# Kernel optimization log

Hardware: AMD Instinct MI355X
Metric: run time of the kernel (lower is better)

Reference implementation:

```python
import jax, jax.numpy as jnp
import numpy as np

M, N = 128, 128          # SOM grid
NITER = 1000             # total training iterations
ALPHA = 0.3              # base learning rate (torch default)
SIGMA = max(M, N) / 2.0  # base neighbourhood radius (torch default)
BS, DIM = 4096, 768


def setup_inputs() -> dict:
    key = jax.random.key(0)
    k1, k2 = jax.random.split(key)
    embedded = jax.random.normal(k1, (BS, DIM), dtype=jnp.float32)   # SapBERT CLS reps
    weights = jax.random.normal(k2, (M * N, DIM), dtype=jnp.float32)  # codebook / SOM weights
    return {"embedded": embedded, "weights": weights, "it": 100}


def reference(embedded, weights, it):
    comps = weights.shape[0]
    # neuron grid locations [comps, 2] (row-major i,j like neuron_locations())
    locs = jnp.stack(
        jnp.meshgrid(jnp.arange(M), jnp.arange(N), indexing="ij"), axis=-1
    ).reshape(comps, 2).astype(jnp.float32)

    # BMU search: squared Euclidean distances (argmin identical to argmin of sqrt)
    # [bs, comps] — avoids materializing the torch [bs, comps, dim] repeat
    d2 = (
        jnp.sum(embedded * embedded, axis=1)[:, None]
        + jnp.sum(weights * weights, axis=1)[None, :]
        - 2.0 * (embedded @ weights.T)
    )
    bmu_index = jnp.argmin(d2, axis=1)          # [bs]
    bmu_loc = locs[bmu_index]                   # [bs, 2] gather

    # linearly decaying learning rate / sigma
    decay = 1.0 - it / NITER
    alpha_op = ALPHA * decay
    sigma_op = SIGMA * decay

    # Gaussian neighbourhood over grid distances [bs, comps]
    grid_d2 = jnp.sum((locs[None, :, :] - bmu_loc[:, None, :]) ** 2, axis=-1)
    lr = alpha_op * jnp.exp(-grid_d2 / (sigma_op * sigma_op))

    # delta[c,d] = sum_b lr[b,c] * (x[b,d] - w[c,d])  (no bs x comps x dim materialization)
    delta = jnp.einsum("bc,bd->cd", lr, embedded) - jnp.sum(lr, axis=0)[:, None] * weights
    return weights + delta
```

## Files before the change

### kernel.cpp

```cpp
#include <hip/hip_runtime.h>
#include <hip/hip_fp16.h>
#include <cstdint>
#include <cstddef>

#define BS    4096
#define DIM   768
#define GM    128
#define GN    128
#define COMPS (GM * GN)
#define NITER_F 1000.0f
#define ALPHA0  0.3f
#define SIGMA0  64.0f

typedef _Float16 half8  __attribute__((ext_vector_type(8)));
typedef _Float16 half4v __attribute__((ext_vector_type(4)));
typedef _Float16 half2v __attribute__((ext_vector_type(2)));
typedef float    floatx4 __attribute__((ext_vector_type(4)));

#define XH_OFF    0UL
#define WH_OFF    (8UL * 1024UL * 1024UL)
#define G_OFF     0UL
#define GH_BYTES  ((size_t)COMPS * DIM * 2UL)
#define BEST_OFF  ((size_t)COMPS * DIM * 4UL)
#define BEST_BYTES ((size_t)BS * 8UL)
#define CNT_OFF   (BEST_OFF + BEST_BYTES)
#define CNT_BYTES ((size_t)COMPS * 4UL)
#define WN2_OFF   (CNT_OFF + CNT_BYTES)

#define GPTR(p) ((const __attribute__((address_space(1))) void*)(p))
#define LPTR(p) ((__attribute__((address_space(3))) void*)(p))

__device__ __forceinline__ unsigned long long packScore(float s, int c) {
    unsigned u = __float_as_uint(s);
    u = (u & 0x80000000u) ? ~u : (u | 0x80000000u);
    return ((unsigned long long)u << 32) | (unsigned)(~(unsigned)c);
}

__device__ __forceinline__ unsigned long long shfl_xor_u64(unsigned long long v, int m) {
    unsigned lo = (unsigned)v, hi = (unsigned)(v >> 32);
    lo = (unsigned)__shfl_xor((int)lo, m, 64);
    hi = (unsigned)__shfl_xor((int)hi, m, 64);
    return ((unsigned long long)hi << 32) | lo;
}

__device__ __forceinline__ void atomicAddPkF16(_Float16* p, half2v v) {
    asm volatile("global_atomic_pk_add_f16 %0, %1, off" : : "v"(p), "v"(v) : "memory");
}

__global__ void cvt_kernel(const float* __restrict__ src, _Float16* __restrict__ dst, int n4) {
    int i = blockIdx.x * 256 + threadIdx.x;
    if (i >= n4) return;
    float4 v = ((const float4*)src)[i];
    half4v h;
    h[0] = (_Float16)v.x; h[1] = (_Float16)v.y;
    h[2] = (_Float16)v.z; h[3] = (_Float16)v.w;
    ((half4v*)dst)[i] = h;
}

__global__ __launch_bounds__(192) void cvtw_wn2_kernel(
    const float* __restrict__ w, _Float16* __restrict__ wh, float* __restrict__ wn2) {
    const int c = blockIdx.x;
    const int t = threadIdx.x;
    const size_t i4 = (size_t)c * 192 + t;
    float4 v = ((const float4*)w)[i4];
    half4v h;
    h[0] = (_Float16)v.x; h[1] = (_Float16)v.y;
    h[2] = (_Float16)v.z; h[3] = (_Float16)v.w;
    ((half4v*)wh)[i4] = h;
    float s = v.x * v.x + v.y * v.y + v.z * v.z + v.w * v.w;
    #pragma unroll
    for (int off = 32; off; off >>= 1) s += __shfl_down(s, off, 64);
    __shared__ float p[3];
    if ((t & 63) == 0) p[t >> 6] = s;
    __syncthreads();
    if (t == 0) wn2[c] = 0.5f * (p[0] + p[1] + p[2]);
}

#define BMU_NT 24

__global__ __launch_bounds__(512, 2) void bmu_kernel(
    const _Float16* __restrict__ xh, const _Float16* __restrict__ wh,
    const float* __restrict__ wn2, unsigned long long* __restrict__ best) {
    __shared__ _Float16 AB[4][2][8192];
    __shared__ unsigned long long red[256];

    const int tid  = threadIdx.x;
    const int wv   = tid >> 6;
    const int lane = tid & 63;
    const int l15  = lane & 15;
    const int q    = lane >> 4;
    const int wr   = wv >> 2;
    const int wc   = wv & 3;

    const int bid = blockIdx.x;
    const int xcd = bid & 7;
    const int rem = bid >> 3;
    const int cbl = rem & 3;
    const int bb  = (rem >> 2) & 15;
    const int cbg = rem >> 6;
    const int cb  = xcd * 8 + cbg * 4 + cbl;
    const int b0 = bb * 256;
    const int c0 = cb * 256;

    if (tid < 256) red[tid] = 0ULL;

    const int Ls = tid >> 3;
    const int ss = tid & 7;
    const int sl = ss ^ (Ls & 7);
    const int prow = 2 * Ls + (sl >> 2);
    const int kc8  = (sl & 3) * 8;
    const _Float16* gA0 = xh + (size_t)(b0 + prow) * DIM + kc8;
    const _Float16* gA1 = gA0 + (size_t)128 * DIM;
    const _Float16* gB0 = wh + (size_t)(c0 + prow) * DIM + kc8;
    const _Float16* gB1 = gB0 + (size_t)128 * DIM;
    const int ldsoff = wv * 512;

    int aoff[8], boff[4];
    #pragma unroll
    for (int i = 0; i < 8; ++i) {
        const int row = wr * 128 + i * 16 + l15;
        const int line = row >> 1;
        const int ps = (((row & 1) << 2) | q) ^ (line & 7);
        aoff[i] = line * 64 + ps * 8;
    }
    #pragma unroll
    for (int jj = 0; jj < 4; ++jj) {
        const int row = wc * 64 + jj * 16 + l15;
        const int line = row >> 1;
        const int ps = (((row & 1) << 2) | q) ^ (line & 7);
        boff[jj] = line * 64 + ps * 8;
    }

    floatx4 acc[8][4];
    #pragma unroll
    for (int i = 0; i < 8; ++i)
        #pragma unroll
        for (int jj = 0; jj < 4; ++jj) acc[i][jj] = (floatx4){0.f, 0.f, 0.f, 0.f};

    #pragma unroll
    for (int t = 0; t < 3; ++t) {
        _Float16* A = &AB[t][0][0];
        _Float16* B = &AB[t][1][0];
        __builtin_amdgcn_global_load_lds(GPTR(gA0 + t * 32), LPTR(A + ldsoff),        16, 0, 0);
        __builtin_amdgcn_global_load_lds(GPTR(gA1 + t * 32), LPTR(A + 4096 + ldsoff), 16, 0, 0);
        __builtin_amdgcn_global_load_lds(GPTR(gB0 + t * 32), LPTR(B + ldsoff),        16, 0, 0);
        __builtin_amdgcn_global_load_lds(GPTR(gB1 + t * 32), LPTR(B + 4096 + ldsoff), 16, 0, 0);
    }

    for (int t = 0; t < BMU_NT; ++t) {
        if (t < BMU_NT - 2)       asm volatile("s_waitcnt vmcnt(8)" ::: "memory");
        else if (t == BMU_NT - 2) asm volatile("s_waitcnt vmcnt(4)" ::: "memory");
        else                      asm volatile("s_waitcnt vmcnt(0)" ::: "memory");
        __builtin_amdgcn_s_barrier();
        asm volatile("" ::: "memory");

        const _Float16* A = &AB[t & 3][0][0];
        const _Float16* B = &AB[t & 3][1][0];
        const bool more = (t + 3) < BMU_NT;
        _Float16* An = &AB[(t + 3) & 3][0][0];
        _Float16* Bn = &AB[(t + 3) & 3][1][0];
        const int t3 = (t + 3) * 32;

        half8 af[8], bf[4];
        #pragma unroll
        for (int i = 0; i < 4; ++i) af[i] = *(const half8*)(A + aoff[i]);
        bf[0] = *(const half8*)(B + boff[0]);
        bf[1] = *(const half8*)(B + boff[1]);
        if (more) __builtin_amdgcn_global_load_lds(GPTR(gA0 + t3), LPTR(An + ldsoff), 16, 0, 0);
        __builtin_amdgcn_s_setprio(1);
        #pragma unroll
        for (int i = 0; i < 4; ++i) {
            acc[i][0] = __builtin_amdgcn_mfma_f32_16x16x32_f16(af[i], bf[0], acc[i][0], 0, 0, 0);
            acc[i][1] = __builtin_amdgcn_mfma_f32_16x16x32_f16(af[i], bf[1], acc[i][1], 0, 0, 0);
        }
        __builtin_amdgcn_s_setprio(0);
        #pragma unroll
        for (int i = 4; i < 8; ++i) af[i] = *(const half8*)(A + aoff[i]);
        if (more) __builtin_amdgcn_global_load_lds(GPTR(gA1 + t3), LPTR(An + 4096 + ldsoff), 16, 0, 0);
        __builtin_amdgcn_s_setprio(1);
        #pragma unroll
        for (int i = 4; i < 8; ++i) {
            acc[i][0] = __builtin_amdgcn_mfma_f32_16x16x32_f16(af[i], bf[0], acc[i][0], 0, 0, 0);
            acc[i][1] = __builtin_amdgcn_mfma_f32_16x16x32_f16(af[i], bf[1], acc[i][1], 0, 0, 0);
        }
        __builtin_amdgcn_s_setprio(0);
        bf[2] = *(const half8*)(B + boff[2]);
        bf[3] = *(const half8*)(B + boff[3]);
        if (more) __builtin_amdgcn_global_load_lds(GPTR(gB0 + t3), LPTR(Bn + ldsoff), 16, 0, 0);
        __builtin_amdgcn_s_setprio(1);
        #pragma unroll
        for (int i = 4; i < 8; ++i) {
            acc[i][2] = __builtin_amdgcn_mfma_f32_16x16x32_f16(af[i], bf[2], acc[i][2], 0, 0, 0);
            acc[i][3] = __builtin_amdgcn_mfma_f32_16x16x32_f16(af[i], bf[3], acc[i][3], 0, 0, 0);
        }
        __builtin_amdgcn_s_setprio(0);
        if (more) __builtin_amdgcn_global_load_lds(GPTR(gB1 + t3), LPTR(Bn + 4096 + ldsoff), 16, 0, 0);
        __builtin_amdgcn_s_setprio(1);
        #pragma unroll
        for (int i = 0; i < 4; ++i) {
            acc[i][2] = __builtin_amdgcn_mfma_f32_16x16x32_f16(af[i], bf[2], acc[i][2], 0, 0, 0);
            acc[i][3] = __builtin_amdgcn_mfma_f32_16x16x32_f16(af[i], bf[3], acc[i][3], 0, 0, 0);
        }
        __builtin_amdgcn_s_setprio(0);
    }

    float wnj[4];
    #pragma unroll
    for (int jj = 0; jj < 4; ++jj) wnj[jj] = wn2[c0 + wc * 64 + jj * 16 + l15];

    #pragma unroll
    for (int i = 0; i < 8; ++i) {
        #pragma unroll
        for (int r = 0; r < 4; ++r) {
            unsigned long long m = 0ULL;
            #pragma unroll
            for (int jj = 0; jj < 4; ++jj) {
                const float s = acc[i][jj][r] - wnj[jj];
                const unsigned long long p = packScore(s, c0 + wc * 64 + jj * 16 + l15);
                if (p > m) m = p;
            }
            #pragma unroll
            for (int msk = 1; msk <= 8; msk <<= 1) {
                const unsigned long long o = shfl_xor_u64(m, msk);
                if (o > m) m = o;
            }
            if (l15 == 0)
                atomicMax(&red[wr * 128 + i * 16 + q * 4 + r], m);
        }
    }
    __syncthreads();
    if (tid < 256) atomicMax(&best[b0 + tid], red[tid]);
}

__global__ void scatter_kernel(const unsigned long long* __restrict__ best,
                               const float* __restrict__ x,
                               _Float16* __restrict__ Gh, float* __restrict__ cnt) {
    const int b = blockIdx.x;
    const int c = (int)(~(unsigned)(best[b] & 0xFFFFFFFFULL));
    _Float16* gr = Gh + (size_t)c * DIM;
    const float2* xr = (const float2*)(x + (size_t)b * DIM);
    #pragma unroll
    for (int u = 0; u < 2; ++u) {
        const int d = threadIdx.x + u * 192;
        const float2 v = xr[d];
        half2v h;
        h[0] = (_Float16)v.x; h[1] = (_Float16)v.y;
        atomicAddPkF16(gr + d * 2, h);
    }
    if (threadIdx.x == 0) atomicAdd(&cnt[c], 1.0f);
}

#define EP 136
#define BP 40

__global__ __launch_bounds__(256) void convA_kernel(
    const _Float16* Gh, _Float16* Hh, const int* __restrict__ itp) {
    __shared__ _Float16 Es[128 * EP];
    __shared__ _Float16 Bs[128 * BP];
    const int d0 = blockIdx.x * 128;
    const int ib = blockIdx.y;
    const int tid = threadIdx.x;
    const int wv = tid >> 6, lane = tid & 63;
    const int l15 = lane & 15, q = lane >> 4;
    const int mrow = (wv >> 1) * 64, ncol = (wv & 1) * 64;

    {
        const float decay = 1.f - (float)(*itp) / NITER_F;
        const float sig = SIGMA0 * decay;
        const float inv = -1.f / (sig * sig);
        const int row = tid >> 1, hh = tid & 1;
        _Float16* dst = Es + row * EP + hh * 64;
        #pragma unroll
        for (int u = 0; u < 64; ++u) {
            const float dd = (float)(row - hh * 64 - u);
            dst[u] = (_Float16)__expf(dd * dd * inv);
        }
    }

    floatx4 acc[4][4];
    #pragma unroll
    for (int i = 0; i < 4; ++i)
        #pragma unroll
        for (int j = 0; j < 4; ++j) acc[i][j] = (floatx4){0.f, 0.f, 0.f, 0.f};

    const int dpo = (tid & 15) * 8;
    const int rsel = tid >> 4;
    const int wsw = ((tid & 15) & 3) << 3;
    for (int k0 = 0; k0 < 128; k0 += 32) {
        __syncthreads();
        #pragma unroll
        for (int s = 0; s < 2; ++s) {
            const int j = k0 + s * 16 + rsel;
            const half8 v = *(const half8*)(Gh + (size_t)(ib * 128 + j) * DIM + d0 + dpo);
            #pragma unroll
            for (int u = 0; u < 8; ++u)
                Bs[(dpo + u) * BP + ((s * 16 + rsel) ^ wsw)] = v[u];
        }
        __syncthreads();
        half8 af[4], bf[4];
        #pragma unroll
        for (int i = 0; i < 4; ++i)
            af[i] = *(const half8*)(Es + (mrow + i * 16 + l15) * EP + k0 + q * 8);
        #pragma unroll
        for (int j = 0; j < 4; ++j) {
            const int row = ncol + j * 16 + l15;
            bf[j] = *(const half8*)(Bs + row * BP + ((q ^ ((row >> 3) & 3)) << 3));
        }
        #pragma unroll
        for (int i = 0; i < 4; ++i)
            #pragma unroll
            for (int j = 0; j < 4; ++j)
                acc[i][j] = __builtin_amdgcn_mfma_f32_16x16x32_f16(af[i], bf[j], acc[i][j], 0, 0, 0);
    }
    __syncthreads();
    float* Ebf = (float*)Es;
    #pragma unroll
    for (int ch = 0; ch < 2; ++ch) {
        if ((wv >> 1) == ch) {
            #pragma unroll
            for (int i = 0; i < 4; ++i)
                #pragma unroll
                for (int j = 0; j < 4; ++j)
                    #pragma unroll
                    for (int r = 0; r < 4; ++r)
                        Ebf[(i * 16 + q * 4 + r) * 132 + ncol + j * 16 + l15] = acc[i][j][r];
        }
        __syncthreads();
        {
            const int row = tid >> 2, seg = tid & 3;
            const int m = ch * 64 + row;
            _Float16* hp = Hh + (size_t)(ib * 128 + m) * DIM + d0 + seg * 32;
            #pragma unroll
            for (int u = 0; u < 4; ++u) {
                const float* sp = Ebf + row * 132 + seg * 32 + u * 8;
                half8 hv;
                #pragma unroll
                for (int e = 0; e < 8; ++e) hv[e] = (_Float16)sp[e];
                *(half8*)(hp + u * 8) = hv;
            }
        }
        __syncthreads();
    }
}

__global__ __launch_bounds__(256) void convB_kernel(
    const _Float16* Hh, const float* __restrict__ w, const float* __restrict__ cnt,
    const int* __restrict__ itp, float* __restrict__ out) {
    __shared__ _Float16 Es[128 * EP];
    __shared__ _Float16 Bs[128 * BP];
    __shared__ float cntHs[128];
    __shared__ float Ss[128];
    const int d0 = blockIdx.x * 128;
    const int jc = blockIdx.y;
    const int tid = threadIdx.x;
    const int wv = tid >> 6, lane = tid & 63;
    const int l15 = lane & 15, q = lane >> 4;
    const int mrow = (wv >> 1) * 64, ncol = (wv & 1) * 64;
    const float decay = 1.f - (float)(*itp) / NITER_F;
    const float alpha = ALPHA0 * decay;
    const float sig = SIGMA0 * decay;
    const float inv = -1.f / (sig * sig);

    if (tid < 128) {
        float s = 0.f;
        for (int j = 0; j < 128; ++j) {
            const float dd = (float)(jc - j);
            s += __expf(dd * dd * inv) * cnt[tid * 128 + j];
        }
        cntHs[tid] = s;
    }
    {
        const int row = tid >> 1, hh = tid & 1;
        _Float16* dst = Es + row * EP + hh * 64;
        #pragma unroll
        for (int u = 0; u < 64; ++u) {
            const float dd = (float)(row - hh * 64 - u);
            dst[u] = (_Float16)__expf(dd * dd * inv);
        }
    }
    __syncthreads();
    if (tid < 128) {
        float s = 0.f;
        for (int i = 0; i < 128; ++i) {
            const float dd = (float)(tid - i);
            s += __expf(dd * dd * inv) * cntHs[i];
        }
        Ss[tid] = s;
    }

    floatx4 acc[4][4];
    #pragma unroll
    for (int i = 0; i < 4; ++i)
        #pragma unroll
        for (int j = 0; j < 4; ++j) acc[i][j] = (floatx4){0.f, 0.f, 0.f, 0.f};

    const int dpo = (tid & 15) * 8;
    const int rsel = tid >> 4;
    const int wsw = ((tid & 15) & 3) << 3;
    for (int k0 = 0; k0 < 128; k0 += 32) {
        __syncthreads();
        #pragma unroll
        for (int s = 0; s < 2; ++s) {
            const int i = k0 + s * 16 + rsel;
            const half8 v = *(const half8*)(Hh + (size_t)(i * 128 + jc) * DIM + d0 + dpo);
            #pragma unroll
            for (int u = 0; u < 8; ++u)
                Bs[(dpo + u) * BP + ((s * 16 + rsel) ^ wsw)] = v[u];
        }
        __syncthreads();
        half8 af[4], bf[4];
        #pragma unroll
        for (int i = 0; i < 4; ++i)
            af[i] = *(const half8*)(Es + (mrow + i * 16 + l15) * EP + k0 + q * 8);
        #pragma unroll
        for (int j = 0; j < 4; ++j) {
            const int row = ncol + j * 16 + l15;
            bf[j] = *(const half8*)(Bs + row * BP + ((q ^ ((row >> 3) & 3)) << 3));
        }
        #pragma unroll
        for (int i = 0; i < 4; ++i)
            #pragma unroll
            for (int j = 0; j < 4; ++j)
                acc[i][j] = __builtin_amdgcn_mfma_f32_16x16x32_f16(af[i], bf[j], acc[i][j], 0, 0, 0);
    }
    __syncthreads();
    float* Ebf = (float*)Es;
    #pragma unroll
    for (int ch = 0; ch < 2; ++ch) {
        if ((wv >> 1) == ch) {
            #pragma unroll
            for (int i = 0; i < 4; ++i)
                #pragma unroll
                for (int j = 0; j < 4; ++j)
                    #pragma unroll
                    for (int r = 0; r < 4; ++r)
                        Ebf[(i * 16 + q * 4 + r) * 132 + ncol + j * 16 + l15] = acc[i][j][r];
        }
        __syncthreads();
        {
            const int row = tid >> 2, seg = tid & 3;
            const int m = ch * 64 + row;
            const int c = m * 128 + jc;
            const float scl = 1.f - alpha * Ss[m];
            const size_t g = (size_t)c * DIM + d0 + seg * 32;
            #pragma unroll
            for (int u = 0; u < 8; ++u) {
                float4 wv4 = *(const float4*)(w + g + u * 4);
                float4 t4  = *(const float4*)(Ebf + row * 132 + seg * 32 + u * 4);
                float4 o;
                o.x = wv4.x * scl + alpha * t4.x;
                o.y = wv4.y * scl + alpha * t4.y;
                o.z = wv4.z * scl + alpha * t4.z;
                o.w = wv4.w * scl + alpha * t4.w;
                *(float4*)(out + g + u * 4) = o;
            }
        }
        __syncthreads();
    }
}

extern "C" void kernel_launch(void* const* d_in, const int* in_sizes, int n_in,
                              void* d_out, int out_size, void* d_ws, size_t ws_size,
                              hipStream_t stream) {
    const float* x  = (const float*)d_in[0];
    const float* w  = (const float*)d_in[1];
    const int* itp  = (const int*)d_in[2];
    float* out = (float*)d_out;
    char* ws = (char*)d_ws;

    _Float16* xh = (_Float16*)(ws + XH_OFF);
    _Float16* wh = (_Float16*)(ws + WH_OFF);
    _Float16* Gh = (_Float16*)(ws + G_OFF);
    unsigned long long* best = (unsigned long long*)(ws + BEST_OFF);
    float* cnt  = (float*)(ws + CNT_OFF);
    float* wn2  = (float*)(ws + WN2_OFF);

    hipMemsetAsync(ws + BEST_OFF, 0, BEST_BYTES + CNT_BYTES, stream);

    cvt_kernel<<<(BS * DIM / 4 + 255) / 256, 256, 0, stream>>>(x, xh, BS * DIM / 4);
    cvtw_wn2_kernel<<<COMPS, 192, 0, stream>>>(w, wh, wn2);

    bmu_kernel<<<dim3(1024), 512, 0, stream>>>(xh, wh, wn2, best);

    hipMemsetAsync(ws + G_OFF, 0, GH_BYTES, stream);
    scatter_kernel<<<BS, 192, 0, stream>>>(best, x, Gh, cnt);

    convA_kernel<<<dim3(6, 128), 256, 0, stream>>>(Gh, Gh, itp);
    convB_kernel<<<dim3(6, 128), 256, 0, stream>>>(Gh, w, cnt, itp, out);
}
```

Measured before the change: 315.6 us.

## Use double-buffered K=64 tiles in BMU GEMM instead of 4-stage K=32

The BMU distance GEMM now loads K-slices of 64 halves per stage into two LDS buffers, where it previously used four buffers of 32. This halves the number of loop iterations and barriers. The LDS row layout and XOR swizzle are changed to match, and each iteration issues twice as many MFMAs. In exchange, prefetch depth drops from three tiles in flight to one, and each iteration waits on vmcnt(0), so global-load latency may be exposed.

```diff
diff --git a/kernel.cpp b/kernel.cpp
--- a/kernel.cpp
+++ b/kernel.cpp
@@ -76,12 +76,12 @@
     if (t == 0) wn2[c] = 0.5f * (p[0] + p[1] + p[2]);
 }
 
-#define BMU_NT 24
+#define BMU_NT 12
 
 __global__ __launch_bounds__(512, 2) void bmu_kernel(
     const _Float16* __restrict__ xh, const _Float16* __restrict__ wh,
     const float* __restrict__ wn2, unsigned long long* __restrict__ best) {
-    __shared__ _Float16 AB[4][2][8192];
+    __shared__ _Float16 AB[2][2][16384];
     __shared__ unsigned long long red[256];
 
     const int tid  = threadIdx.x;
@@ -104,31 +104,29 @@
 
     if (tid < 256) red[tid] = 0ULL;
 
-    const int Ls = tid >> 3;
-    const int ss = tid & 7;
-    const int sl = ss ^ (Ls & 7);
-    const int prow = 2 * Ls + (sl >> 2);
-    const int kc8  = (sl & 3) * 8;
-    const _Float16* gA0 = xh + (size_t)(b0 + prow) * DIM + kc8;
-    const _Float16* gA1 = gA0 + (size_t)128 * DIM;
-    const _Float16* gB0 = wh + (size_t)(c0 + prow) * DIM + kc8;
-    const _Float16* gB1 = gB0 + (size_t)128 * DIM;
+    const int rowi = tid >> 3;
+    const int ss   = tid & 7;
+    const int sl   = ss ^ (rowi & 7);
+    const _Float16* gA0 = xh + (size_t)(b0 +   0 + rowi) * DIM + sl * 8;
+    const _Float16* gA1 = xh + (size_t)(b0 +  64 + rowi) * DIM + sl * 8;
+    const _Float16* gA2 = xh + (size_t)(b0 + 128 + rowi) * DIM + sl * 8;
+    const _Float16* gA3 = xh + (size_t)(b0 + 192 + rowi) * DIM + sl * 8;
+    const _Float16* gB0 = wh + (size_t)(c0 +   0 + rowi) * DIM + sl * 8;
+    const _Float16* gB1 = wh + (size_t)(c0 +  64 + rowi) * DIM + sl * 8;
+    const _Float16* gB2 = wh + (size_t)(c0 + 128 + rowi) * DIM + sl * 8;
+    const _Float16* gB3 = wh + (size_t)(c0 + 192 + rowi) * DIM + sl * 8;
     const int ldsoff = wv * 512;
 
     int aoff[8], boff[4];
     #pragma unroll
     for (int i = 0; i < 8; ++i) {
         const int row = wr * 128 + i * 16 + l15;
-        const int line = row >> 1;
-        const int ps = (((row & 1) << 2) | q) ^ (line & 7);
-        aoff[i] = line * 64 + ps * 8;
+        aoff[i] = row * 64 + (q ^ (row & 7)) * 8;
     }
     #pragma unroll
     for (int jj = 0; jj < 4; ++jj) {
         const int row = wc * 64 + jj * 16 + l15;
-        const int line = row >> 1;
-        const int ps = (((row & 1) << 2) | q) ^ (line & 7);
-        boff[jj] = line * 64 + ps * 8;
+        boff[jj] = row * 64 + (q ^ (row & 7)) * 8;
     }
 
     floatx4 acc[8][4];
@@ -137,36 +135,37 @@
         #pragma unroll
         for (int jj = 0; jj < 4; ++jj) acc[i][jj] = (floatx4){0.f, 0.f, 0.f, 0.f};
 
-    #pragma unroll
-    for (int t = 0; t < 3; ++t) {
-        _Float16* A = &AB[t][0][0];
-        _Float16* B = &AB[t][1][0];
-        __builtin_amdgcn_global_load_lds(GPTR(gA0 + t * 32), LPTR(A + ldsoff),        16, 0, 0);
-        __builtin_amdgcn_global_load_lds(GPTR(gA1 + t * 32), LPTR(A + 4096 + ldsoff), 16, 0, 0);
-        __builtin_amdgcn_global_load_lds(GPTR(gB0 + t * 32), LPTR(B + ldsoff),        16, 0, 0);
-        __builtin_amdgcn_global_load_lds(GPTR(gB1 + t * 32), LPTR(B + 4096 + ldsoff), 16, 0, 0);
+    {
+        _Float16* A = &AB[0][0][0];
+        _Float16* B = &AB[0][1][0];
+        __builtin_amdgcn_global_load_lds(GPTR(gA0), LPTR(A +     0 + ldsoff), 16, 0, 0);
+        __builtin_amdgcn_global_load_lds(GPTR(gA1), LPTR(A +  4096 + ldsoff), 16, 0, 0);
+        __builtin_amdgcn_global_load_lds(GPTR(gA2), LPTR(A +  8192 + ldsoff), 16, 0, 0);
+        __builtin_amdgcn_global_load_lds(GPTR(gA3), LPTR(A + 12288 + ldsoff), 16, 0, 0);
+        __builtin_amdgcn_global_load_lds(GPTR(gB0), LPTR(B +     0 + ldsoff), 16, 0, 0);
+        __builtin_amdgcn_global_load_lds(GPTR(gB1), LPTR(B +  4096 + ldsoff), 16, 0, 0);
+        __builtin_amdgcn_global_load_lds(GPTR(gB2), LPTR(B +  8192 + ldsoff), 16, 0, 0);
+        __builtin_amdgcn_global_load_lds(GPTR(gB3), LPTR(B + 12288 + ldsoff), 16, 0, 0);
     }
 
     for (int t = 0; t < BMU_NT; ++t) {
-        if (t < BMU_NT - 2)       asm volatile("s_waitcnt vmcnt(8)" ::: "memory");
-        else if (t == BMU_NT - 2) asm volatile("s_waitcnt vmcnt(4)" ::: "memory");
-        else                      asm volatile("s_waitcnt vmcnt(0)" ::: "memory");
+        asm volatile("s_waitcnt vmcnt(0)" ::: "memory");
         __builtin_amdgcn_s_barrier();
         asm volatile("" ::: "memory");
 
-        const _Float16* A = &AB[t & 3][0][0];
-        const _Float16* B = &AB[t & 3][1][0];
-        const bool more = (t + 3) < BMU_NT;
-        _Float16* An = &AB[(t + 3) & 3][0][0];
-        _Float16* Bn = &AB[(t + 3) & 3][1][0];
-        const int t3 = (t + 3) * 32;
+        const _Float16* A = &AB[t & 1][0][0];
+        const _Float16* B = &AB[t & 1][1][0];
+        const bool more = (t + 1) < BMU_NT;
+        _Float16* An = &AB[(t + 1) & 1][0][0];
+        _Float16* Bn = &AB[(t + 1) & 1][1][0];
+        const int tk = (t + 1) * 64;
 
         half8 af[8], bf[4];
         #pragma unroll
         for (int i = 0; i < 4; ++i) af[i] = *(const half8*)(A + aoff[i]);
         bf[0] = *(const half8*)(B + boff[0]);
         bf[1] = *(const half8*)(B + boff[1]);
-        if (more) __builtin_amdgcn_global_load_lds(GPTR(gA0 + t3), LPTR(An + ldsoff), 16, 0, 0);
+        if (more) __builtin_amdgcn_global_load_lds(GPTR(gA0 + tk), LPTR(An + 0 + ldsoff), 16, 0, 0);
         __builtin_amdgcn_s_setprio(1);
         #pragma unroll
         for (int i = 0; i < 4; ++i) {
@@ -176,7 +175,7 @@
         __builtin_amdgcn_s_setprio(0);
         #pragma unroll
         for (int i = 4; i < 8; ++i) af[i] = *(const half8*)(A + aoff[i]);
-        if (more) __builtin_amdgcn_global_load_lds(GPTR(gA1 + t3), LPTR(An + 4096 + ldsoff), 16, 0, 0);
+        if (more) __builtin_amdgcn_global_load_lds(GPTR(gA1 + tk), LPTR(An + 4096 + ldsoff), 16, 0, 0);
         __builtin_amdgcn_s_setprio(1);
         #pragma unroll
         for (int i = 4; i < 8; ++i) {
@@ -186,7 +185,7 @@
         __builtin_amdgcn_s_setprio(0);
         bf[2] = *(const half8*)(B + boff[2]);
         bf[3] = *(const half8*)(B + boff[3]);
-        if (more) __builtin_amdgcn_global_load_lds(GPTR(gB0 + t3), LPTR(Bn + ldsoff), 16, 0, 0);
+        if (more) __builtin_amdgcn_global_load_lds(GPTR(gA2 + tk), LPTR(An + 8192 + ldsoff), 16, 0, 0);
         __builtin_amdgcn_s_setprio(1);
         #pragma unroll
         for (int i = 4; i < 8; ++i) {
@@ -194,7 +193,47 @@
             acc[i][3] = __builtin_amdgcn_mfma_f32_16x16x32_f16(af[i], bf[3], acc[i][3], 0, 0, 0);
         }
         __builtin_amdgcn_s_setprio(0);
-        if (more) __builtin_amdgcn_global_load_lds(GPTR(gB1 + t3), LPTR(Bn + 4096 + ldsoff), 16, 0, 0);
+        if (more) __builtin_amdgcn_global_load_lds(GPTR(gA3 + tk), LPTR(An + 12288 + ldsoff), 16, 0, 0);
+        __builtin_amdgcn_s_setprio(1);
+        #pragma unroll
+        for (int i = 0; i < 4; ++i) {
+            acc[i][2] = __builtin_amdgcn_mfma_f32_16x16x32_f16(af[i], bf[2], acc[i][2], 0, 0, 0);
+            acc[i][3] = __builtin_amdgcn_mfma_f32_16x16x32_f16(af[i], bf[3], acc[i][3], 0, 0, 0);
+        }
+        __builtin_amdgcn_s_setprio(0);
+        #pragma unroll
+        for (int i = 0; i < 4; ++i) af[i] = *(const half8*)(A + (aoff[i] ^ 32));
+        bf[0] = *(const half8*)(B + (boff[0] ^ 32));
+        bf[1] = *(const half8*)(B + (boff[1] ^ 32));
+        if (more) __builtin_amdgcn_global_load_lds(GPTR(gB0 + tk), LPTR(Bn + 0 + ldsoff), 16, 0, 0);
+        __builtin_amdgcn_s_setprio(1);
+        #pragma unroll
+        for (int i = 0; i < 4; ++i) {
+            acc[i][0] = __builtin_amdgcn_mfma_f32_16x16x32_f16(af[i], bf[0], acc[i][0], 0, 0, 0);
+            acc[i][1] = __builtin_amdgcn_mfma_f32_16x16x32_f16(af[i], bf[1], acc[i][1], 0, 0, 0);
+        }
+        __builtin_amdgcn_s_setprio(0);
+        #pragma unroll
+        for (int i = 4; i < 8; ++i) af[i] = *(const half8*)(A + (aoff[i] ^ 32));
+        if (more) __builtin_amdgcn_global_load_lds(GPTR(gB1 + tk), LPTR(Bn + 4096 + ldsoff), 16, 0, 0);
+        __builtin_amdgcn_s_setprio(1);
+        #pragma unroll
+        for (int i = 4; i < 8; ++i) {
+            acc[i][0] = __builtin_amdgcn_mfma_f32_16x16x32_f16(af[i], bf[0], acc[i][0], 0, 0, 0);
+            acc[i][1] = __builtin_amdgcn_mfma_f32_16x16x32_f16(af[i], bf[1], acc[i][1], 0, 0, 0);
+        }
+        __builtin_amdgcn_s_setprio(0);
+        bf[2] = *(const half8*)(B + (boff[2] ^ 32));
+        bf[3] = *(const half8*)(B + (boff[3] ^ 32));
+        if (more) __builtin_amdgcn_global_load_lds(GPTR(gB2 + tk), LPTR(Bn + 8192 + ldsoff), 16, 0, 0);
+        __builtin_amdgcn_s_setprio(1);
+        #pragma unroll
+        for (int i = 4; i < 8; ++i) {
+            acc[i][2] = __builtin_amdgcn_mfma_f32_16x16x32_f16(af[i], bf[2], acc[i][2], 0, 0, 0);
+            acc[i][3] = __builtin_amdgcn_mfma_f32_16x16x32_f16(af[i], bf[3], acc[i][3], 0, 0, 0);
+        }
+        __builtin_amdgcn_s_setprio(0);
+        if (more) __builtin_amdgcn_global_load_lds(GPTR(gB3 + tk), LPTR(Bn + 12288 + ldsoff), 16, 0, 0);
         __builtin_amdgcn_s_setprio(1);
         #pragma unroll
         for (int i = 0; i < 4; ++i) {
```

New measurement: 315.1 us. About the same (-0.2%).
